# Optimization experiments

Hardware: AMD Instinct MI355X
Metric: run time of the kernel (lower is better)

## Reference

```python
import jax, jax.numpy as jnp
import numpy as np

B, N, D, H, E = 4, 2048, 512, 8, 512   # batch, seq, d_model, heads, dpb_embedding
D1 = 2 * D                              # expand_ratio * d_model (multiple of H)
HD = D1 // H                            # head dim for v/u space
GAMMA = 0.999


def _srms(x):
    # SimpleRMSNorm: x / (||x|| * d^-0.5 + eps)
    return x / (jnp.sqrt(jnp.mean(jnp.square(x), axis=-1, keepdims=True)) + 1e-8)


def setup_inputs() -> dict:
    key = jax.random.key(0)
    ks = jax.random.split(key, 10)
    s = 0.02

    def lin(k, i, o):
        kw, kb = jax.random.split(k)
        return (jax.random.normal(kw, (i, o), jnp.float32) * s,
                jax.random.normal(kb, (o,), jnp.float32) * s)

    Wu, bu = lin(ks[0], D, D1)
    Wv, bv = lin(ks[1], D, D1)
    Wo, bo = lin(ks[2], D1, D)
    Wp, bp = lin(ks[3], 1, E)        # DPB pos_proj: scalar position -> dpb_dim
    W1, b1 = lin(ks[4], E, E)
    W2, b2 = lin(ks[5], E, E)
    W3, b3 = lin(ks[6], E, E)
    Wz, bz = lin(ks[7], E, H * HD)   # DPB out: dpb_dim -> h*head_dim
    x = jax.random.normal(ks[8], (B, N, D), jnp.float32)
    return dict(x=x, Wu=Wu, bu=bu, Wv=Wv, bv=bv, Wo=Wo, bo=bo,
                Wp=Wp, bp=bp, W1=W1, b1=b1, W2=W2, b2=b2, W3=W3, b3=b3,
                Wz=Wz, bz=bz)


def reference(x, Wu, bu, Wv, bv, Wo, bo, Wp, bp, W1, b1, W2, b2, W3, b3, Wz, bz):
    shortcut = x                       # token_shift_type=-1, resi_param=False
    xn = _srms(x)                      # pre_norm = SimpleRMSNorm(d_model)
    u = jax.nn.silu(xn @ Wu + bu)      # b n d1
    v = jax.nn.silu(xn @ Wv + bv)      # b n d1
    b, n, _ = x.shape
    v = v.reshape(b, n, H, HD).transpose(0, 2, 1, 3)   # b h n d

    # --- DPB (Rpe MLP) on positions [0, 1, ..., n-1]; row 0 is the zero lag ---
    pos = jnp.arange(0, n, dtype=x.dtype).reshape(n, 1)  # par_type=1
    hcf = pos @ Wp + bp
    for W, bb in ((W1, b1), (W2, b2), (W3, b3)):         # non-residual layers
        hcf = jax.nn.relu(_srms(hcf)) @ W + bb
    coef = jax.nn.relu(_srms(hcf)) @ Wz + bz             # n, h*d
    coef = coef.reshape(n, H, HD).transpose(1, 0, 2)     # h n d
    zero = coef[:, :1]                                   # h 1 d  (lag 0)
    posc = coef[:, 1:]                                   # h n-1 d (lags 1..n-1)

    # fixed exponential decay gamma^i on positive lags (use_decay=True)
    decay = GAMMA ** jnp.arange(1, n, dtype=x.dtype)[None, :, None]
    # causal: negative lags are zero; rfft zero-pads to 2n
    a = jnp.concatenate([zero, decay * posc, zero], axis=1)  # h, n+1, d

    # --- causal Toeplitz matmul as circular conv of length 2n ---
    m = 2 * n
    fv = jnp.fft.rfft(v, m, axis=2)           # b h m/2+1 d
    fa = jnp.fft.rfft(a, m, axis=1)[None]     # 1 h m/2+1 d
    out = jnp.fft.irfft(fv * fa, m, axis=2)[:, :, :n]  # b h n d

    out = out.transpose(0, 2, 1, 3).reshape(b, n, H * HD)  # b n d1
    out = u * out                               # u-gating
    return out @ Wo + bo + shortcut             # output proj + residual
```

## Files before the change

### kernel.cpp

```cpp
#include <hip/hip_runtime.h>
#include <hip/hip_bf16.h>
#include <math.h>

using bf16 = __hip_bfloat16;
typedef short bf16x8 __attribute__((ext_vector_type(8)));
typedef float f32x4 __attribute__((ext_vector_type(4)));

#define GAMMA_LOG2 (-0.0014434688536725045f)

union Bf16Bits { bf16 h; unsigned short s; };
union VecU { uint4 q; unsigned short s[8]; };

__device__ inline unsigned short bf16_bits(float z)
{
    Bf16Bits u;
    u.h = __float2bfloat16(z);
    return u.s;
}

__device__ inline unsigned int packbf2(float a, float b)
{
    return (unsigned int)bf16_bits(a) | ((unsigned int)bf16_bits(b) << 16);
}

__device__ __forceinline__ void async_copy16(unsigned short* lds, const bf16* g)
{
    __builtin_amdgcn_global_load_lds(
        (const __attribute__((address_space(1))) unsigned int*)(const void*)g,
        (__attribute__((address_space(3))) unsigned int*)(void*)lds,
        16, 0, 0);
}

struct PrepArgs {
    const float* src[3];
    bf16* dst[3];
    int R[3];
    int C[3];
    int pfx[4];
};

__global__ void k_prep(PrepArgs pa)
{
    __shared__ float tile[32][33];
    int bid = blockIdx.x;
    int seg = 0;
    while (bid >= pa.pfx[seg + 1]) ++seg;
    int local = bid - pa.pfx[seg];
    int R = pa.R[seg], C = pa.C[seg];
    int ctiles = C >> 5;
    int c0 = (local % ctiles) * 32, r0 = (local / ctiles) * 32;
    const float* in = pa.src[seg];
    bf16* out = pa.dst[seg];
    int tx = threadIdx.x & 31, ty = threadIdx.x >> 5;
#pragma unroll
    for (int i = 0; i < 4; ++i) {
        int r = r0 + ty + 8 * i;
        tile[ty + 8 * i][tx] = in[(size_t)r * C + c0 + tx];
    }
    __syncthreads();
#pragma unroll
    for (int i = 0; i < 4; ++i) {
        int cc = c0 + ty + 8 * i, rr = r0 + tx;
        out[(size_t)cc * R + rr] = __float2bfloat16(tile[tx][ty + 8 * i]);
    }
}

__global__ void k_prep_mlp(const float* __restrict__ W1, const float* __restrict__ W2,
                           const float* __restrict__ W3, const float* __restrict__ Wz,
                           bf16* __restrict__ Wf)
{
    int g = blockIdx.x * 256 + threadIdx.x;
    int unit = g >> 15;
    int idx = g & 32767;
    int lane = idx & 63;
    int nj = (idx >> 6) & 7;
    int ks = (idx >> 9) & 15;
    int wc = idx >> 13;
    int lm = lane & 15, lq = lane >> 4;
    int k0 = ks * 32 + lq * 8;
    const float* src;
    int N, o;
    if (unit < 3) {
        src = (unit == 0) ? W1 : (unit == 1) ? W2 : W3;
        N = 512;
        o = wc * 128 + nj * 16 + lm;
    } else {
        src = Wz;
        N = 1024;
        o = (unit - 3) * 512 + wc * 128 + nj * 16 + lm;
    }
    VecU v;
#pragma unroll
    for (int j = 0; j < 8; ++j)
        v.s[j] = bf16_bits(src[(size_t)(k0 + j) * N + o]);
    *(uint4*)(void*)(Wf + (size_t)g * 8) = v.q;
}

__global__ void k_transpose5(const bf16* __restrict__ uvb, const bf16* __restrict__ ab,
                             bf16* __restrict__ vtb, bf16* __restrict__ atb)
{
    __shared__ unsigned short tile[64][65];
    const int z = blockIdx.z;
    const bf16* in;
    bf16* out;
    int in_stride, col0;
    if (z < 4) {
        in = uvb + (size_t)z * 2048 * 2048;
        out = vtb + (size_t)z * 1024 * 2048;
        in_stride = 2048;
        col0 = 1024;
    } else {
        in = ab;
        out = atb;
        in_stride = 1024;
        col0 = 0;
    }
    const int t = threadIdx.x;
    int c0 = blockIdx.x * 64, r0 = blockIdx.y * 64;
#pragma unroll
    for (int it = 0; it < 2; ++it) {
        int r = it * 32 + (t >> 3), cc = (t & 7) * 8;
        VecU v;
        v.q = *(const uint4*)(const void*)(in + (size_t)(r0 + r) * in_stride + col0 + c0 + cc);
#pragma unroll
        for (int i = 0; i < 8; ++i) tile[r][cc + i] = v.s[i];
    }
    __syncthreads();
#pragma unroll
    for (int it = 0; it < 2; ++it) {
        int c = it * 32 + (t >> 3), rr = (t & 7) * 8;
        VecU v;
#pragma unroll
        for (int i = 0; i < 8; ++i) v.s[i] = tile[rr + i][c];
        *(uint4*)(void*)(out + (size_t)(c0 + c) * 2048 + r0 + rr) = v.q;
    }
}

__global__ void k_gate_transpose(const bf16* __restrict__ ud1t, const bf16* __restrict__ uv,
                                 bf16* __restrict__ out)
{
    __shared__ float tile[32][33];
    const int b = blockIdx.z;
    int c0 = blockIdx.x * 32, t0 = blockIdx.y * 32;
    int tx = threadIdx.x & 31, ty = threadIdx.x >> 5;
#pragma unroll
    for (int i = 0; i < 4; ++i) {
        int cc = c0 + ty + 8 * i;
        tile[ty + 8 * i][tx] = __bfloat162float(ud1t[((size_t)b * 1024 + cc) * 2048 + t0 + tx]);
    }
    __syncthreads();
#pragma unroll
    for (int i = 0; i < 4; ++i) {
        int t = t0 + ty + 8 * i, c = c0 + tx;
        float u = __bfloat162float(uv[((size_t)b * 2048 + t) * 2048 + c]);
        out[((size_t)b * 2048 + t) * 1024 + c] = __float2bfloat16(tile[tx][ty + 8 * i] * u);
    }
}

__global__ void k_rms_x(const float* __restrict__ x, bf16* __restrict__ xn)
{
    int row = blockIdx.x, t = threadIdx.x;
    const float* xr = x + (size_t)row * 512;
    float a = xr[t], b = xr[t + 256];
    float v = a * a + b * b;
#pragma unroll
    for (int m = 32; m >= 1; m >>= 1) v += __shfl_xor(v, m, 64);
    __shared__ float ws[4];
    if ((t & 63) == 0) ws[t >> 6] = v;
    __syncthreads();
    float tot = ws[0] + ws[1] + ws[2] + ws[3];
    float s = 1.f / (sqrtf(tot * (1.f / 512.f)) + 1e-8f);
    bf16* o = xn + (size_t)row * 512;
    o[t] = __float2bfloat16(a * s);
    o[t + 256] = __float2bfloat16(b * s);
}

struct SharedUV {
    union {
        struct { unsigned short AB[2][2][128 * 32]; } g;
        struct {
            unsigned short X[32][520];
            float sq[16][17];
            float red[4][32];
            float scale[32];
        } m;
    };
};

__global__ __launch_bounds__(256, 2) void k_uv_mlp(
    const bf16* __restrict__ A, const bf16* __restrict__ Bt,
    const float* __restrict__ bu, const float* __restrict__ bv,
    const float* __restrict__ Wp, const float* __restrict__ bp,
    const bf16* __restrict__ Wf,
    const float* __restrict__ b1, const float* __restrict__ b2,
    const float* __restrict__ b3, const float* __restrict__ bz,
    bf16* __restrict__ uvb, bf16* __restrict__ ab)
{
    __shared__ SharedUV sh;

    const int tid = threadIdx.x, lane = tid & 63, w = tid >> 6;
    const int lm = lane & 15, lq = lane >> 4;

    if (blockIdx.x < 64) {
        unsigned short (&X)[32][520] = sh.m.X;
        float (&sq)[16][17] = sh.m.sq;
        float (&red)[4][32] = sh.m.red;
        float (&scale)[32] = sh.m.scale;

        const int posBase = blockIdx.x * 32;

#pragma unroll
        for (int hf = 0; hf < 2; ++hf) {
            const int rl = tid >> 4;
            const int r = hf * 16 + rl;
            const int c0 = (tid & 15) * 32;
            float vals[32];
            float ssq = 0.f;
            const float fp = (float)(posBase + r);
#pragma unroll
            for (int e = 0; e < 32; ++e) {
                float z = fp * Wp[c0 + e] + bp[c0 + e];
                vals[e] = z;
                ssq += z * z;
            }
            sq[rl][tid & 15] = ssq;
            __syncthreads();
            float tot = 0.f;
#pragma unroll
            for (int i = 0; i < 16; ++i) tot += sq[rl][i];
            float s = 1.f / (sqrtf(tot * (1.f / 512.f)) + 1e-8f);
            unsigned int* xrow = (unsigned int*)&X[r][c0];
#pragma unroll
            for (int e = 0; e < 16; ++e)
                xrow[e] = packbf2(fmaxf(vals[2 * e] * s, 0.f), fmaxf(vals[2 * e + 1] * s, 0.f));
            __syncthreads();
        }

        auto layer_mm = [&](const bf16* Wu_, f32x4 (&acc)[2][8]) {
            const bf16* base = Wu_ + (size_t)w * 65536 + (size_t)lane * 8;
            bf16x8 bufB[2][8];
#pragma unroll
            for (int nj = 0; nj < 8; ++nj)
                bufB[0][nj] = *(const bf16x8*)(const void*)(base + nj * 512);
#pragma unroll
            for (int ks = 0; ks < 16; ++ks) {
                const int cb = ks & 1;
                if (ks < 15) {
#pragma unroll
                    for (int nj = 0; nj < 8; ++nj)
                        bufB[cb ^ 1][nj] = *(const bf16x8*)(const void*)(base + (ks + 1) * 4096 + nj * 512);
                }
                bf16x8 af0 = *(const bf16x8*)(const void*)&X[lm][ks * 32 + lq * 8];
                bf16x8 af1 = *(const bf16x8*)(const void*)&X[16 + lm][ks * 32 + lq * 8];
#pragma unroll
                for (int nj = 0; nj < 8; ++nj) {
                    acc[0][nj] = __builtin_amdgcn_mfma_f32_16x16x32_bf16(af0, bufB[cb][nj], acc[0][nj], 0, 0, 0);
                    acc[1][nj] = __builtin_amdgcn_mfma_f32_16x16x32_bf16(af1, bufB[cb][nj], acc[1][nj], 0, 0, 0);
                }
            }
        };

        const float* bs[3] = {b1, b2, b3};
        for (int l = 0; l < 3; ++l) {
            f32x4 acc[2][8];
#pragma unroll
            for (int mi = 0; mi < 2; ++mi)
#pragma unroll
                for (int i = 0; i < 8; ++i) acc[mi][i] = (f32x4){0.f, 0.f, 0.f, 0.f};
            layer_mm(Wf + (size_t)l * 262144, acc);
#pragma unroll
            for (int mi = 0; mi < 2; ++mi)
#pragma unroll
                for (int nj = 0; nj < 8; ++nj) {
                    float bb = bs[l][w * 128 + nj * 16 + lm];
#pragma unroll
                    for (int r = 0; r < 4; ++r) acc[mi][nj][r] += bb;
                }
            float pr[2][4] = {{0.f, 0.f, 0.f, 0.f}, {0.f, 0.f, 0.f, 0.f}};
#pragma unroll
            for (int mi = 0; mi < 2; ++mi)
#pragma unroll
                for (int nj = 0; nj < 8; ++nj)
#pragma unroll
                    for (int r = 0; r < 4; ++r) pr[mi][r] += acc[mi][nj][r] * acc[mi][nj][r];
#pragma unroll
            for (int m = 1; m < 16; m <<= 1)
#pragma unroll
                for (int mi = 0; mi < 2; ++mi)
#pragma unroll
                    for (int r = 0; r < 4; ++r) pr[mi][r] += __shfl_xor(pr[mi][r], m);
            if (lm == 0)
#pragma unroll
                for (int mi = 0; mi < 2; ++mi)
#pragma unroll
                    for (int r = 0; r < 4; ++r) red[w][mi * 16 + lq * 4 + r] = pr[mi][r];
            __syncthreads();
            if (tid < 32) {
                float tot = red[0][tid] + red[1][tid] + red[2][tid] + red[3][tid];
                scale[tid] = 1.f / (sqrtf(tot * (1.f / 512.f)) + 1e-8f);
            }
            __syncthreads();
#pragma unroll
            for (int mi = 0; mi < 2; ++mi)
#pragma unroll
                for (int nj = 0; nj < 8; ++nj) {
                    int col = w * 128 + nj * 16 + lm;
#pragma unroll
                    for (int r = 0; r < 4; ++r) {
                        int row = mi * 16 + lq * 4 + r;
                        float z = fmaxf(acc[mi][nj][r] * scale[row], 0.f);
                        *(unsigned short*)&X[row][col] = bf16_bits(z);
                    }
                }
            __syncthreads();
        }

#pragma unroll
        for (int h = 0; h < 2; ++h) {
            f32x4 acc[2][8];
#pragma unroll
            for (int mi = 0; mi < 2; ++mi)
#pragma unroll
                for (int i = 0; i < 8; ++i) acc[mi][i] = (f32x4){0.f, 0.f, 0.f, 0.f};
            layer_mm(Wf + (size_t)(3 + h) * 262144, acc);
#pragma unroll
            for (int mi = 0; mi < 2; ++mi)
#pragma unroll
                for (int nj = 0; nj < 8; ++nj) {
                    int col = h * 512 + w * 128 + nj * 16 + lm;
                    float bb = bz[col];
#pragma unroll
                    for (int r = 0; r < 4; ++r) {
                        int pos = posBase + mi * 16 + lq * 4 + r;
                        float z = (acc[mi][nj][r] + bb) * exp2f((float)pos * GAMMA_LOG2);
                        ab[(size_t)pos * 1024 + col] = __float2bfloat16(z);
                    }
                }
        }
        return;
    }

    unsigned short (&AB)[2][2][128 * 32] = sh.g.AB;

    const int gid = (int)blockIdx.x - 64;
    const int wm = (w >> 1) * 64, wn = (w & 1) * 64;
    const long rowBase = (long)(gid & 63) * 128, colBase = (long)(gid >> 6) * 128;

    const int srow = tid >> 2;
    const int sqz  = (tid & 3) ^ ((srow >> 1) & 3);
    const bf16* gA  = A  + (rowBase + srow) * 512 + sqz * 8;
    const bf16* gB  = Bt + (colBase + srow) * 512 + sqz * 8;
    const bf16* gA2 = gA + (size_t)64 * 512;
    const bf16* gB2 = gB + (size_t)64 * 512;
    const int ls0 = w * 512;
    const int ls1 = 2048 + w * 512;

    const int rdA = ((wm + lm) * 4 + (lq ^ ((lm >> 1) & 3))) * 8;
    const int rdB = ((wn + lm) * 4 + (lq ^ ((lm >> 1) & 3))) * 8;

    f32x4 acc[4][4];
    f32x4 zz = {0.f, 0.f, 0.f, 0.f};
#pragma unroll
    for (int i = 0; i < 4; ++i)
#pragma unroll
        for (int j = 0; j < 4; ++j) acc[i][j] = zz;

    async_copy16(&AB[0][0][ls0], gA);
    async_copy16(&AB[0][0][ls1], gA2);
    async_copy16(&AB[0][1][ls0], gB);
    async_copy16(&AB[0][1][ls1], gB2);
    __syncthreads();

#pragma unroll
    for (int t = 0; t < 16; ++t) {
        const int cur = t & 1;
        if (t < 15) {
            const int kk = (t + 1) * 32;
            async_copy16(&AB[cur ^ 1][0][ls0], gA + kk);
            async_copy16(&AB[cur ^ 1][0][ls1], gA2 + kk);
            async_copy16(&AB[cur ^ 1][1][ls0], gB + kk);
            async_copy16(&AB[cur ^ 1][1][ls1], gB2 + kk);
        }
        bf16x8 af[4], bfr[4];
#pragma unroll
        for (int mi = 0; mi < 4; ++mi)
            af[mi] = *(const bf16x8*)(const void*)&AB[cur][0][rdA + mi * 512];
#pragma unroll
        for (int nj = 0; nj < 4; ++nj)
            bfr[nj] = *(const bf16x8*)(const void*)&AB[cur][1][rdB + nj * 512];
#pragma unroll
        for (int mi = 0; mi < 4; ++mi)
#pragma unroll
            for (int nj = 0; nj < 4; ++nj)
                acc[mi][nj] = __builtin_amdgcn_mfma_f32_16x16x32_bf16(af[mi], bfr[nj], acc[mi][nj], 0, 0, 0);
        if (t < 15) __syncthreads();
    }

#pragma unroll
    for (int mi = 0; mi < 4; ++mi)
#pragma unroll
        for (int nj = 0; nj < 4; ++nj) {
            long col = colBase + wn + nj * 16 + lm;
            float bb = (col < 1024) ? bu[col] : bv[col - 1024];
#pragma unroll
            for (int r = 0; r < 4; ++r) {
                long row = rowBase + wm + mi * 16 + lq * 4 + r;
                float z = acc[mi][nj][r] + bb;
                z = z / (1.f + __expf(-z));
                uvb[(size_t)row * 2048 + col] = __float2bfloat16(z);
            }
        }
}

template <int BM, int BN, int WM, int WN>
__global__ __launch_bounds__(256, 2) void k_gemm_out(
    const bf16* __restrict__ A, const bf16* __restrict__ Bt,
    const float* __restrict__ bias0, const float* __restrict__ addsrc,
    float* __restrict__ outp, int M, int N, int K)
{
    constexpr int BK = 32, LDT = BK + 8;
    constexpr int MI = WM / 16, NJ = WN / 16;
    constexpr int WCOLS = BN / WN;
    __shared__ unsigned short As[BM * LDT];
    __shared__ unsigned short Bs[BN * LDT];
    const int tid = threadIdx.x;
    const int lane = tid & 63, w = tid >> 6;
    const int wm = (w / WCOLS) * WM, wn = (w % WCOLS) * WN;
    const int lm = lane & 15, lq = lane >> 4;
    const long rowBase = (long)blockIdx.x * BM, colBase = (long)blockIdx.y * BN;

    f32x4 acc[MI][NJ];
    f32x4 zz = {0.f, 0.f, 0.f, 0.f};
#pragma unroll
    for (int i = 0; i < MI; ++i)
#pragma unroll
        for (int j = 0; j < NJ; ++j) acc[i][j] = zz;

    for (int k0 = 0; k0 < K; k0 += BK) {
#pragma unroll
        for (int i = 0; i < BM / 64; ++i) {
            int idx = (i * 256 + tid) * 8;
            int r = idx >> 5, kk = idx & 31;
            *(uint4*)(void*)(As + r * LDT + kk) =
                *(const uint4*)(const void*)(A + (rowBase + r) * K + k0 + kk);
        }
#pragma unroll
        for (int i = 0; i < BN / 64; ++i) {
            int idx = (i * 256 + tid) * 8;
            int r = idx >> 5, kk = idx & 31;
            *(uint4*)(void*)(Bs + r * LDT + kk) =
                *(const uint4*)(const void*)(Bt + (colBase + r) * K + k0 + kk);
        }
        __syncthreads();
        bf16x8 af[MI], bfr[NJ];
#pragma unroll
        for (int mi = 0; mi < MI; ++mi)
            af[mi] = *(const bf16x8*)(const void*)(As + (wm + mi * 16 + lm) * LDT + lq * 8);
#pragma unroll
        for (int nj = 0; nj < NJ; ++nj)
            bfr[nj] = *(const bf16x8*)(const void*)(Bs + (wn + nj * 16 + lm) * LDT + lq * 8);
#pragma unroll
        for (int mi = 0; mi < MI; ++mi)
#pragma unroll
            for (int nj = 0; nj < NJ; ++nj)
                acc[mi][nj] = __builtin_amdgcn_mfma_f32_16x16x32_bf16(af[mi], bfr[nj], acc[mi][nj], 0, 0, 0);
        __syncthreads();
    }

#pragma unroll
    for (int mi = 0; mi < MI; ++mi)
#pragma unroll
        for (int nj = 0; nj < NJ; ++nj) {
            long col = colBase + wn + nj * 16 + lm;
#pragma unroll
            for (int r = 0; r < 4; ++r) {
                long row = rowBase + wm + mi * 16 + lq * 4 + r;
                size_t off = (size_t)row * N + col;
                outp[off] = acc[mi][nj][r] + bias0[col] + addsrc[off];
            }
        }
}

__global__ __launch_bounds__(256, 4) void k_conv_mfma(
    const bf16* __restrict__ vt, const bf16* __restrict__ at, bf16* __restrict__ ud1t)
{
    __shared__ unsigned short ash2[2][2068];
    __shared__ unsigned short vsh[4][3072];

    const int tid = threadIdx.x, lane = tid & 63, w = tid >> 6;
    const int c = blockIdx.x;

    {
        const unsigned short* asrc = (const unsigned short*)(at + (size_t)c * 2048);
        for (int i = tid; i < 2068; i += 256) {
#pragma unroll
            for (int k = 0; k < 2; ++k) {
                int src = 2047 - i - k;
                ash2[k][i] = (src >= 0) ? asrc[src] : (unsigned short)0;
            }
        }
    }
    {
        const bf16* vsrc = vt + ((size_t)w * 1024 + c) * 2048;
#pragma unroll
        for (int q = 0; q < 4; ++q) {
            int li = q * 64 + lane;
            int tile = li >> 1, hf = li & 1;
            *(uint4*)(void*)&vsh[w][tile * 24 + hf * 8] =
                *(const uint4*)(const void*)(vsrc + li * 8);
        }
    }
    __syncthreads();

    const int lm = lane & 15, lq = lane >> 4;
    const int h = lq >> 1, p0 = (lq & 1) * 8;
    const int kcopy = (lm + 1) & 1;
    const int base = 31 - 16 * h - lm + p0 - kcopy;
    const unsigned int* aw = (const unsigned int*)(void*)&ash2[kcopy][0] + (base >> 1);
    const unsigned short* vw = &vsh[w][0];

    f32x4 acc[8];
    f32x4 zz = {0.f, 0.f, 0.f, 0.f};
#pragma unroll
    for (int i = 0; i < 8; ++i) acc[i] = zz;
    const bf16x8 zfrag = (bf16x8)(short)0;

    for (int d2 = 0; d2 < 16; d2 += 2) {
        bf16x8 vf[8];
        const int tb = lm - d2 - h;
        {
            int T = tb > 0 ? tb : 0;
            bf16x8 f = *(const bf16x8*)(const void*)(vw + T * 24 + p0);
            vf[0] = (tb < 0) ? zfrag : f;
        }
#pragma unroll
        for (int dl = 1; dl < 8; ++dl)
            vf[dl] = *(const bf16x8*)(const void*)(vw + (dl * 16 + tb) * 24 + p0);

#pragma unroll
        for (int dt = 0; dt < 8; ++dt) {
            const int m16 = (63 - ((dt * 16 + d2) >> 1)) * 16;
            union { unsigned int u[4]; bf16x8 v; } af;
            af.u[0] = aw[m16 + 0];
            af.u[1] = aw[m16 + 1];
            af.u[2] = aw[m16 + 2];
            af.u[3] = aw[m16 + 3];
#pragma unroll
            for (int dl = 0; dl < 8 - dt; ++dl)
                acc[dt + dl] = __builtin_amdgcn_mfma_f32_16x16x32_bf16(af.v, vf[dl], acc[dt + dl], 0, 0, 0);
        }
    }

    __syncthreads();
    float* stg = (float*)(void*)((char*)(void*)&ash2[0][0] + w * 1024);
    bf16* dst = ud1t + ((size_t)w * 1024 + c) * 2048;
#pragma unroll
    for (int jg = 0; jg < 8; ++jg) {
        *(f32x4*)(void*)&stg[lm * 16 + lq * 4] = acc[jg];
        f32x4 vv = *(const f32x4*)(const void*)&stg[lane * 4];
        uint2 o;
        o.x = packbf2(vv.x, vv.y);
        o.y = packbf2(vv.z, vv.w);
        *(uint2*)(void*)(dst + jg * 256 + lane * 4) = o;
    }
}

extern "C" void kernel_launch(void* const* d_in, const int* in_sizes, int n_in,
                              void* d_out, int out_size, void* d_ws, size_t ws_size,
                              hipStream_t stream)
{
    const float* x  = (const float*)d_in[0];
    const float* Wu = (const float*)d_in[1];
    const float* bu = (const float*)d_in[2];
    const float* Wv = (const float*)d_in[3];
    const float* bv = (const float*)d_in[4];
    const float* Wo = (const float*)d_in[5];
    const float* bo = (const float*)d_in[6];
    const float* Wp = (const float*)d_in[7];
    const float* bp = (const float*)d_in[8];
    const float* W1 = (const float*)d_in[9];
    const float* b1 = (const float*)d_in[10];
    const float* W2 = (const float*)d_in[11];
    const float* b2 = (const float*)d_in[12];
    const float* W3 = (const float*)d_in[13];
    const float* b3 = (const float*)d_in[14];
    const float* Wz = (const float*)d_in[15];
    const float* bz = (const float*)d_in[16];

    char* p = (char*)d_ws;
    auto carve = [&](size_t bytes) { void* q = (void*)p; p += (bytes + 255) & ~(size_t)255; return q; };
    bf16*  xn   = (bf16*)carve((size_t)8192 * 512 * 2);
    bf16*  Wuvt = (bf16*)carve((size_t)2048 * 512 * 2);
    bf16*  Wot  = (bf16*)carve((size_t)512 * 1024 * 2);
    bf16*  Wf   = (bf16*)carve((size_t)5 * 262144 * 2);
    bf16*  uvb  = (bf16*)carve((size_t)8192 * 2048 * 2);
    bf16*  ud1  = (bf16*)carve((size_t)8192 * 1024 * 2);
    bf16*  ab   = (bf16*)carve((size_t)2048 * 1024 * 2);
    bf16*  vtb  = (bf16*)carve((size_t)4 * 1024 * 2048 * 2);
    bf16*  atb  = (bf16*)carve((size_t)1024 * 2048 * 2);
    bf16*  ud1t = (bf16*)carve((size_t)4 * 1024 * 2048 * 2);

    PrepArgs pa;
    const float* srcs[3] = {Wu, Wv, Wo};
    bf16* dsts[3] = {Wuvt, Wuvt + (size_t)1024 * 512, Wot};
    int Rs[3] = {512, 512, 1024};
    int Cs[3] = {1024, 1024, 512};
    int acc_t = 0;
    for (int i = 0; i < 3; ++i) {
        pa.src[i] = srcs[i]; pa.dst[i] = dsts[i]; pa.R[i] = Rs[i]; pa.C[i] = Cs[i];
        pa.pfx[i] = acc_t;
        acc_t += (Rs[i] / 32) * (Cs[i] / 32);
    }
    pa.pfx[3] = acc_t;
    k_prep<<<acc_t, 256, 0, stream>>>(pa);

    k_prep_mlp<<<640, 256, 0, stream>>>(W1, W2, W3, Wz, Wf);

    k_rms_x<<<8192, 256, 0, stream>>>(x, xn);

    k_uv_mlp<<<1088, 256, 0, stream>>>(xn, Wuvt, bu, bv, Wp, bp,
                                       Wf, b1, b2, b3, bz, uvb, ab);

    k_transpose5<<<dim3(16, 32, 5), 256, 0, stream>>>(uvb, ab, vtb, atb);

    k_conv_mfma<<<dim3(1024), 256, 0, stream>>>(vtb, atb, ud1t);

    k_gate_transpose<<<dim3(32, 64, 4), 256, 0, stream>>>(ud1t, uvb, ud1);

    k_gemm_out<128, 128, 64, 64><<<dim3(64, 4), 256, 0, stream>>>(
        ud1, Wot, bo, x, (float*)d_out, 8192, 512, 1024);
}
```

Baseline: 250.3 us.

## Split fused UV GEMM and DPB MLP kernel into separate launches

Separates the combined kernel, which branched on block index between the DPB MLP path and the u/v projection GEMM, into two kernels with their own launch bounds. The GEMM kernel can now target higher occupancy, with a min-blocks hint of 4, without sharing the MLP branch's register and LDS footprint. The MLP kernel deepens its weight prefetch from double to quad buffering. The cost is an extra launch and the loss of overlap between the 64 MLP blocks and the GEMM blocks, since the MLP now runs serially before the GEMM on the same stream.

```diff
diff --git a/kernel.cpp b/kernel.cpp
--- a/kernel.cpp
+++ b/kernel.cpp
@@ -175,174 +175,165 @@
     o[t + 256] = __float2bfloat16(b * s);
 }
 
-struct SharedUV {
-    union {
-        struct { unsigned short AB[2][2][128 * 32]; } g;
-        struct {
-            unsigned short X[32][520];
-            float sq[16][17];
-            float red[4][32];
-            float scale[32];
-        } m;
-    };
-};
-
-__global__ __launch_bounds__(256, 2) void k_uv_mlp(
-    const bf16* __restrict__ A, const bf16* __restrict__ Bt,
-    const float* __restrict__ bu, const float* __restrict__ bv,
+__global__ __launch_bounds__(256, 1) void k_mlp(
     const float* __restrict__ Wp, const float* __restrict__ bp,
     const bf16* __restrict__ Wf,
     const float* __restrict__ b1, const float* __restrict__ b2,
     const float* __restrict__ b3, const float* __restrict__ bz,
-    bf16* __restrict__ uvb, bf16* __restrict__ ab)
-{
-    __shared__ SharedUV sh;
+    bf16* __restrict__ ab)
+{
+    __shared__ unsigned short X[32][520];
+    __shared__ float sq[16][17];
+    __shared__ float red[4][32];
+    __shared__ float scale[32];
 
     const int tid = threadIdx.x, lane = tid & 63, w = tid >> 6;
     const int lm = lane & 15, lq = lane >> 4;
-
-    if (blockIdx.x < 64) {
-        unsigned short (&X)[32][520] = sh.m.X;
-        float (&sq)[16][17] = sh.m.sq;
-        float (&red)[4][32] = sh.m.red;
-        float (&scale)[32] = sh.m.scale;
-
-        const int posBase = blockIdx.x * 32;
-
-#pragma unroll
-        for (int hf = 0; hf < 2; ++hf) {
-            const int rl = tid >> 4;
-            const int r = hf * 16 + rl;
-            const int c0 = (tid & 15) * 32;
-            float vals[32];
-            float ssq = 0.f;
-            const float fp = (float)(posBase + r);
-#pragma unroll
-            for (int e = 0; e < 32; ++e) {
-                float z = fp * Wp[c0 + e] + bp[c0 + e];
-                vals[e] = z;
-                ssq += z * z;
-            }
-            sq[rl][tid & 15] = ssq;
-            __syncthreads();
-            float tot = 0.f;
-#pragma unroll
-            for (int i = 0; i < 16; ++i) tot += sq[rl][i];
-            float s = 1.f / (sqrtf(tot * (1.f / 512.f)) + 1e-8f);
-            unsigned int* xrow = (unsigned int*)&X[r][c0];
-#pragma unroll
-            for (int e = 0; e < 16; ++e)
-                xrow[e] = packbf2(fmaxf(vals[2 * e] * s, 0.f), fmaxf(vals[2 * e + 1] * s, 0.f));
-            __syncthreads();
-        }
-
-        auto layer_mm = [&](const bf16* Wu_, f32x4 (&acc)[2][8]) {
-            const bf16* base = Wu_ + (size_t)w * 65536 + (size_t)lane * 8;
-            bf16x8 bufB[2][8];
+    const int posBase = blockIdx.x * 32;
+
+#pragma unroll
+    for (int hf = 0; hf < 2; ++hf) {
+        const int rl = tid >> 4;
+        const int r = hf * 16 + rl;
+        const int c0 = (tid & 15) * 32;
+        float vals[32];
+        float ssq = 0.f;
+        const float fp = (float)(posBase + r);
+#pragma unroll
+        for (int e = 0; e < 32; ++e) {
+            float z = fp * Wp[c0 + e] + bp[c0 + e];
+            vals[e] = z;
+            ssq += z * z;
+        }
+        sq[rl][tid & 15] = ssq;
+        __syncthreads();
+        float tot = 0.f;
+#pragma unroll
+        for (int i = 0; i < 16; ++i) tot += sq[rl][i];
+        float s = 1.f / (sqrtf(tot * (1.f / 512.f)) + 1e-8f);
+        unsigned int* xrow = (unsigned int*)&X[r][c0];
+#pragma unroll
+        for (int e = 0; e < 16; ++e)
+            xrow[e] = packbf2(fmaxf(vals[2 * e] * s, 0.f), fmaxf(vals[2 * e + 1] * s, 0.f));
+        __syncthreads();
+    }
+
+    auto layer_mm = [&](const bf16* Wu_, f32x4 (&acc)[2][8]) {
+        const bf16* base = Wu_ + (size_t)w * 65536 + (size_t)lane * 8;
+        bf16x8 bufB[4][8];
+#pragma unroll
+        for (int d = 0; d < 3; ++d)
 #pragma unroll
             for (int nj = 0; nj < 8; ++nj)
-                bufB[0][nj] = *(const bf16x8*)(const void*)(base + nj * 512);
-#pragma unroll
-            for (int ks = 0; ks < 16; ++ks) {
-                const int cb = ks & 1;
-                if (ks < 15) {
-#pragma unroll
-                    for (int nj = 0; nj < 8; ++nj)
-                        bufB[cb ^ 1][nj] = *(const bf16x8*)(const void*)(base + (ks + 1) * 4096 + nj * 512);
+                bufB[d][nj] = *(const bf16x8*)(const void*)(base + d * 4096 + nj * 512);
+#pragma unroll
+        for (int ks = 0; ks < 16; ++ks) {
+            const int cb = ks & 3;
+            if (ks < 13) {
+                const int pf = (ks + 3) & 3;
+#pragma unroll
+                for (int nj = 0; nj < 8; ++nj)
+                    bufB[pf][nj] = *(const bf16x8*)(const void*)(base + (ks + 3) * 4096 + nj * 512);
+            }
+            bf16x8 af0 = *(const bf16x8*)(const void*)&X[lm][ks * 32 + lq * 8];
+            bf16x8 af1 = *(const bf16x8*)(const void*)&X[16 + lm][ks * 32 + lq * 8];
+#pragma unroll
+            for (int nj = 0; nj < 8; ++nj) {
+                acc[0][nj] = __builtin_amdgcn_mfma_f32_16x16x32_bf16(af0, bufB[cb][nj], acc[0][nj], 0, 0, 0);
+                acc[1][nj] = __builtin_amdgcn_mfma_f32_16x16x32_bf16(af1, bufB[cb][nj], acc[1][nj], 0, 0, 0);
+            }
+        }
+    };
+
+    const float* bs[3] = {b1, b2, b3};
+    for (int l = 0; l < 3; ++l) {
+        f32x4 acc[2][8];
+#pragma unroll
+        for (int mi = 0; mi < 2; ++mi)
+#pragma unroll
+            for (int i = 0; i < 8; ++i) acc[mi][i] = (f32x4){0.f, 0.f, 0.f, 0.f};
+        layer_mm(Wf + (size_t)l * 262144, acc);
+#pragma unroll
+        for (int mi = 0; mi < 2; ++mi)
+#pragma unroll
+            for (int nj = 0; nj < 8; ++nj) {
+                float bb = bs[l][w * 128 + nj * 16 + lm];
+#pragma unroll
+                for (int r = 0; r < 4; ++r) acc[mi][nj][r] += bb;
+            }
+        float pr[2][4] = {{0.f, 0.f, 0.f, 0.f}, {0.f, 0.f, 0.f, 0.f}};
+#pragma unroll
+        for (int mi = 0; mi < 2; ++mi)
+#pragma unroll
+            for (int nj = 0; nj < 8; ++nj)
+#pragma unroll
+                for (int r = 0; r < 4; ++r) pr[mi][r] += acc[mi][nj][r] * acc[mi][nj][r];
+#pragma unroll
+        for (int m = 1; m < 16; m <<= 1)
+#pragma unroll
+            for (int mi = 0; mi < 2; ++mi)
+#pragma unroll
+                for (int r = 0; r < 4; ++r) pr[mi][r] += __shfl_xor(pr[mi][r], m);
+        if (lm == 0)
+#pragma unroll
+            for (int mi = 0; mi < 2; ++mi)
+#pragma unroll
+                for (int r = 0; r < 4; ++r) red[w][mi * 16 + lq * 4 + r] = pr[mi][r];
+        __syncthreads();
+        if (tid < 32) {
+            float tot = red[0][tid] + red[1][tid] + red[2][tid] + red[3][tid];
+            scale[tid] = 1.f / (sqrtf(tot * (1.f / 512.f)) + 1e-8f);
+        }
+        __syncthreads();
+#pragma unroll
+        for (int mi = 0; mi < 2; ++mi)
+#pragma unroll
+            for (int nj = 0; nj < 8; ++nj) {
+                int col = w * 128 + nj * 16 + lm;
+#pragma unroll
+                for (int r = 0; r < 4; ++r) {
+                    int row = mi * 16 + lq * 4 + r;
+                    float z = fmaxf(acc[mi][nj][r] * scale[row], 0.f);
+                    *(unsigned short*)&X[row][col] = bf16_bits(z);
                 }
-                bf16x8 af0 = *(const bf16x8*)(const void*)&X[lm][ks * 32 + lq * 8];
-                bf16x8 af1 = *(const bf16x8*)(const void*)&X[16 + lm][ks * 32 + lq * 8];
-#pragma unroll
-                for (int nj = 0; nj < 8; ++nj) {
-                    acc[0][nj] = __builtin_amdgcn_mfma_f32_16x16x32_bf16(af0, bufB[cb][nj], acc[0][nj], 0, 0, 0);
-                    acc[1][nj] = __builtin_amdgcn_mfma_f32_16x16x32_bf16(af1, bufB[cb][nj], acc[1][nj], 0, 0, 0);
+            }
+        __syncthreads();
+    }
+
+#pragma unroll
+    for (int h = 0; h < 2; ++h) {
+        f32x4 acc[2][8];
+#pragma unroll
+        for (int mi = 0; mi < 2; ++mi)
+#pragma unroll
+            for (int i = 0; i < 8; ++i) acc[mi][i] = (f32x4){0.f, 0.f, 0.f, 0.f};
+        layer_mm(Wf + (size_t)(3 + h) * 262144, acc);
+#pragma unroll
+        for (int mi = 0; mi < 2; ++mi)
+#pragma unroll
+            for (int nj = 0; nj < 8; ++nj) {
+                int col = h * 512 + w * 128 + nj * 16 + lm;
+                float bb = bz[col];
+#pragma unroll
+                for (int r = 0; r < 4; ++r) {
+                    int pos = posBase + mi * 16 + lq * 4 + r;
+                    float z = (acc[mi][nj][r] + bb) * exp2f((float)pos * GAMMA_LOG2);
+                    ab[(size_t)pos * 1024 + col] = __float2bfloat16(z);
                 }
             }
-        };
-
-        const float* bs[3] = {b1, b2, b3};
-        for (int l = 0; l < 3; ++l) {
-            f32x4 acc[2][8];
-#pragma unroll
-            for (int mi = 0; mi < 2; ++mi)
-#pragma unroll
-                for (int i = 0; i < 8; ++i) acc[mi][i] = (f32x4){0.f, 0.f, 0.f, 0.f};
-            layer_mm(Wf + (size_t)l * 262144, acc);
-#pragma unroll
-            for (int mi = 0; mi < 2; ++mi)
-#pragma unroll
-                for (int nj = 0; nj < 8; ++nj) {
-                    float bb = bs[l][w * 128 + nj * 16 + lm];
-#pragma unroll
-                    for (int r = 0; r < 4; ++r) acc[mi][nj][r] += bb;
-                }
-            float pr[2][4] = {{0.f, 0.f, 0.f, 0.f}, {0.f, 0.f, 0.f, 0.f}};
-#pragma unroll
-            for (int mi = 0; mi < 2; ++mi)
-#pragma unroll
-                for (int nj = 0; nj < 8; ++nj)
-#pragma unroll
-                    for (int r = 0; r < 4; ++r) pr[mi][r] += acc[mi][nj][r] * acc[mi][nj][r];
-#pragma unroll
-            for (int m = 1; m < 16; m <<= 1)
-#pragma unroll
-                for (int mi = 0; mi < 2; ++mi)
-#pragma unroll
-                    for (int r = 0; r < 4; ++r) pr[mi][r] += __shfl_xor(pr[mi][r], m);
-            if (lm == 0)
-#pragma unroll
-                for (int mi = 0; mi < 2; ++mi)
-#pragma unroll
-                    for (int r = 0; r < 4; ++r) red[w][mi * 16 + lq * 4 + r] = pr[mi][r];
-            __syncthreads();
-            if (tid < 32) {
-                float tot = red[0][tid] + red[1][tid] + red[2][tid] + red[3][tid];
-                scale[tid] = 1.f / (sqrtf(tot * (1.f / 512.f)) + 1e-8f);
-            }
-            __syncthreads();
-#pragma unroll
-            for (int mi = 0; mi < 2; ++mi)
-#pragma unroll
-                for (int nj = 0; nj < 8; ++nj) {
-                    int col = w * 128 + nj * 16 + lm;
-#pragma unroll
-                    for (int r = 0; r < 4; ++r) {
-                        int row = mi * 16 + lq * 4 + r;
-                        float z = fmaxf(acc[mi][nj][r] * scale[row], 0.f);
-                        *(unsigned short*)&X[row][col] = bf16_bits(z);
-                    }
-                }
-            __syncthreads();
-        }
-
-#pragma unroll
-        for (int h = 0; h < 2; ++h) {
-            f32x4 acc[2][8];
-#pragma unroll
-            for (int mi = 0; mi < 2; ++mi)
-#pragma unroll
-                for (int i = 0; i < 8; ++i) acc[mi][i] = (f32x4){0.f, 0.f, 0.f, 0.f};
-            layer_mm(Wf + (size_t)(3 + h) * 262144, acc);
-#pragma unroll
-            for (int mi = 0; mi < 2; ++mi)
-#pragma unroll
-                for (int nj = 0; nj < 8; ++nj) {
-                    int col = h * 512 + w * 128 + nj * 16 + lm;
-                    float bb = bz[col];
-#pragma unroll
-                    for (int r = 0; r < 4; ++r) {
-                        int pos = posBase + mi * 16 + lq * 4 + r;
-                        float z = (acc[mi][nj][r] + bb) * exp2f((float)pos * GAMMA_LOG2);
-                        ab[(size_t)pos * 1024 + col] = __float2bfloat16(z);
-                    }
-                }
-        }
-        return;
-    }
-
-    unsigned short (&AB)[2][2][128 * 32] = sh.g.AB;
-
-    const int gid = (int)blockIdx.x - 64;
+    }
+}
+
+__global__ __launch_bounds__(256, 4) void k_uv(
+    const bf16* __restrict__ A, const bf16* __restrict__ Bt,
+    const float* __restrict__ bu, const float* __restrict__ bv,
+    bf16* __restrict__ uvb)
+{
+    __shared__ unsigned short AB[2][2][128 * 32];
+
+    const int tid = threadIdx.x, lane = tid & 63, w = tid >> 6;
+    const int lm = lane & 15, lq = lane >> 4;
+    const int gid = blockIdx.x;
     const int wm = (w >> 1) * 64, wn = (w & 1) * 64;
     const long rowBase = (long)(gid & 63) * 128, colBase = (long)(gid >> 6) * 128;
 
@@ -618,8 +609,9 @@
 
     k_rms_x<<<8192, 256, 0, stream>>>(x, xn);
 
-    k_uv_mlp<<<1088, 256, 0, stream>>>(xn, Wuvt, bu, bv, Wp, bp,
-                                       Wf, b1, b2, b3, bz, uvb, ab);
+    k_mlp<<<64, 256, 0, stream>>>(Wp, bp, Wf, b1, b2, b3, bz, ab);
+
+    k_uv<<<1024, 256, 0, stream>>>(xn, Wuvt, bu, bv, uvb);
 
     k_transpose5<<<dim3(16, 32, 5), 256, 0, stream>>>(uvb, ab, vtb, atb);
 
```

Measured after the change: 286.7 us. +14.5%, slower.
